# Optimization experiments

Hardware: AMD Instinct MI355X
Metric: run time of the kernel (lower is better)

The kernel has to match this reference:

```python
import jax, jax.numpy as jnp
import numpy as np

B, S, H, DH = 1, 4096, 8, 40  # hardcoded in the original forward
D = H * DH  # 320

def setup_inputs() -> dict:
    key = jax.random.key(0)
    ks = jax.random.split(key, 6)
    s = 1.0 / np.sqrt(D)
    return {
        "x": jax.random.normal(ks[0], (B, S, D), dtype=jnp.float32),
        "Wq": jax.random.normal(ks[1], (D, D), dtype=jnp.float32) * s,
        "Wk": jax.random.normal(ks[2], (D, D), dtype=jnp.float32) * s,
        "Wv": jax.random.normal(ks[3], (D, D), dtype=jnp.float32) * s,
        "Wo": jax.random.normal(ks[4], (D, D), dtype=jnp.float32) * s,
        "bo": jnp.zeros((D,), dtype=jnp.float32),
    }

def reference(x, Wq, Wk, Wv, Wo, bo):
    scale = DH ** (-0.5)
    # nn.Linear(bias=False): y = x @ W^T. context = x (self-attention).
    q = x @ Wq.T
    k = x @ Wk.T
    v = x @ Wv.T
    # split heads: [B,S,D] -> [B*H, S, DH]
    def split_heads(t):
        return t.reshape(B, S, H, DH).transpose(0, 2, 1, 3).reshape(B * H, S, DH)
    q, k, v = split_heads(q), split_heads(k), split_heads(v)
    # fp32 QK^T (original forces float), softmax, AV
    sim = jnp.einsum('bid,bjd->bij', q.astype(jnp.float32), k.astype(jnp.float32)) * scale
    attn = jax.nn.softmax(sim, axis=-1)
    out = jnp.einsum('bij,bjd->bid', attn, v)
    # merge heads: [B*H, S, DH] -> [B, S, D]
    out = out.reshape(B, H, S, DH).transpose(0, 2, 1, 3).reshape(B, S, D)
    return out @ Wo.T + bo
```

## Files before the change

kernel.cpp:

```cpp
#include <hip/hip_runtime.h>
#include <math.h>


#define NS 4096
#define ND 320
#define SCALE2 0.2281101152f
#define HS48 196608
#define VTH 163840
#define XN 1310720

#define KSTR 56
#define VSTR 72
#define VB   3584
#define BUF  7040

typedef __attribute__((ext_vector_type(8))) short bf16x8;
typedef __attribute__((ext_vector_type(16))) float f32x16;

static __device__ __forceinline__ unsigned short f2bru(float f) {
  return (unsigned short)((__builtin_bit_cast(unsigned int, f) + 0x8000u) >> 16);
}
static __device__ __forceinline__ unsigned int pk2ru(float a, float b) {
  unsigned int ua = __builtin_bit_cast(unsigned int, a) + 0x8000u;
  unsigned int ub = __builtin_bit_cast(unsigned int, b) + 0x8000u;
  return __builtin_amdgcn_perm(ub, ua, 0x07060302u);
}
static __device__ __forceinline__ unsigned int pk2t(float a, float b) {
  return __builtin_amdgcn_perm(__builtin_bit_cast(unsigned int, b),
                               __builtin_bit_cast(unsigned int, a), 0x07060302u);
}
static __device__ __forceinline__ float fexp2(float x) {
  return __builtin_amdgcn_exp2f(x);
}
static __device__ __forceinline__ bf16x8 ld8a(const unsigned short* p) {
  return __builtin_bit_cast(bf16x8, *(const uint4*)p);
}
static __device__ __forceinline__ void st16a(unsigned short* p, uint4 v) {
  *(uint4*)p = v;
}
static __device__ __forceinline__ uint4 ld16u(const unsigned short* p) {
  uint2 a = *(const uint2*)p, b = *(const uint2*)(p + 4);
  return make_uint4(a.x, a.y, b.x, b.y);
}
static __device__ __forceinline__ void st16(unsigned short* p, uint4 v) {
  *(uint2*)p = make_uint2(v.x, v.y);
  *(uint2*)(p + 4) = make_uint2(v.z, v.w);
}
static __device__ __forceinline__ int sig32(int q) {
  int s = q >> 4, h2 = (q >> 3) & 1, j = q & 7;
  return (s << 4) | ((j >> 2) << 3) | (h2 << 2) | (j & 3);
}

__global__ __launch_bounds__(256) void proj_qkv_kernel(
    const float* __restrict__ x, const float* __restrict__ Wq,
    const float* __restrict__ Wk, const float* __restrict__ Wv,
    unsigned short* __restrict__ Qp, unsigned short* __restrict__ Kp,
    unsigned short* __restrict__ Vt) {
  const int zi = blockIdx.y;
  const int z = zi / 5;
  const int bnn = (zi - z * 5) * 64;
  const float* W = (z == 0) ? Wq : (z == 1) ? Wk : Wv;
  __shared__ __align__(16) unsigned short As[64 * 88];
  __shared__ __align__(16) unsigned short Bs[64 * 88];
  const int t = threadIdx.x;
  const int w = t >> 6, l = t & 63, l31 = l & 31, hi = l >> 5;
  const int bm = blockIdx.x * 64;
  const int m0 = (w >> 1) * 32, n0 = (w & 1) * 32;
  f32x16 acc = {0,0,0,0,0,0,0,0,0,0,0,0,0,0,0,0};
  const unsigned short* af = As + (m0 + l31) * 88 + hi * 8;
  const unsigned short* bf = Bs + (n0 + l31) * 88 + hi * 8;
  for (int k0 = 0; k0 < ND; k0 += 64) {
    __syncthreads();
#pragma unroll
    for (int i = 0; i < 2; i++) {
      int c = t + i * 256;
      int row = c >> 3, kc = (c & 7) << 3;
      const float* g = x + (bm + row) * ND + k0 + kc;
      float4 v0 = *(const float4*)g, v1 = *(const float4*)(g + 4);
      st16a(As + row * 88 + kc,
            make_uint4(pk2ru(v0.x, v0.y), pk2ru(v0.z, v0.w),
                       pk2ru(v1.x, v1.y), pk2ru(v1.z, v1.w)));
    }
#pragma unroll
    for (int i = 0; i < 2; i++) {
      int c = t + i * 256;
      int row = c >> 3, kc = (c & 7) << 3;
      const float* g = W + (bnn + row) * ND + k0 + kc;
      float4 v0 = *(const float4*)g, v1 = *(const float4*)(g + 4);
      st16a(Bs + row * 88 + kc,
            make_uint4(pk2ru(v0.x, v0.y), pk2ru(v0.z, v0.w),
                       pk2ru(v1.x, v1.y), pk2ru(v1.z, v1.w)));
    }
    __syncthreads();
#pragma unroll
    for (int ks = 0; ks < 4; ks++) {
      acc = __builtin_amdgcn_mfma_f32_32x32x16_bf16(
          ld8a(af + ks * 16), ld8a(bf + ks * 16), acc, 0, 0, 0);
    }
  }
  __syncthreads();
  if (z < 2) {
    unsigned short* Tile = As;
    unsigned short* Y = (z == 0) ? Qp : Kp;
    const float sc = (z == 0) ? SCALE2 : 1.0f;
    const unsigned int padw = (z == 0) ? 0xC200u : 0x3F80u;
#pragma unroll
    for (int r2 = 0; r2 < 16; r2++) {
      int lr = m0 + (r2 & 3) + 8 * (r2 >> 2) + 4 * hi;
      Tile[lr * 68 + n0 + l31] = f2bru(acc[r2] * sc);
    }
    __syncthreads();
#pragma unroll
    for (int i = 0; i < 2; i++) {
      int c = t + i * 256;
      int row = c >> 3, ch = c & 7;
      int j = bnn + ch * 8;
      int h = j / 40, dh = j - h * 40;
      uint4 v = ld16u(Tile + row * 68 + ch * 8);
      st16(Y + h * HS48 + (bm + row) * 48 + dh, v);
      if (dh == 0)
        st16(Y + h * HS48 + (bm + row) * 48 + 40, make_uint4(padw, 0u, 0u, 0u));
    }
  } else {
    unsigned short* Tile = As;
#pragma unroll
    for (int r2 = 0; r2 < 16; r2++) {
      int lr = m0 + (r2 & 3) + 8 * (r2 >> 2) + 4 * hi;
      Tile[(n0 + l31) * 68 + lr] = f2bru(acc[r2]);
    }
    __syncthreads();
#pragma unroll
    for (int i = 0; i < 2; i++) {
      int c = t + i * 256;
      int row = c >> 3, ch = c & 7;
      int j = bnn + row;
      int h = j / 40, dd = j - h * 40;
      uint4 v = ld16u(Tile + row * 68 + ch * 8);
      st16(Vt + h * VTH + dd * NS + bm + ch * 8, v);
    }
  }
}

__global__ __launch_bounds__(256, 4) void attn_kernel(
    const unsigned short* __restrict__ Qp, const unsigned short* __restrict__ Kp,
    const unsigned short* __restrict__ Vt, unsigned short* __restrict__ Op,
    float* __restrict__ Lp) {
  const int b = blockIdx.x;
  const int h = b & 7, ks = (b >> 3) & 3, qt = b >> 5;
  const int t = threadIdx.x;
  const int w = t >> 6, l = t & 63, l31 = l & 31, hi = l >> 5;
  __shared__ __align__(16) unsigned short Lds[2 * BUF];
  for (int i = t; i < 576; i += 256) {
    int bsel = (i >= 288) ? 1 : 0;
    int ui = i - bsel * 288;
    int rr = ui / 36, cc = ui - rr * 36;
    ((unsigned int*)Lds)[bsel * (BUF / 2) + (VB / 2) + (40 + rr) * 36 + cc] =
        (rr == 0 && cc < 32) ? 0x3F803F80u : 0u;
  }

  const int kbase = ks * 1024;
  const int qbase = qt * 128 + w * 32;
  const unsigned short* qp = Qp + h * HS48 + (qbase + l31) * 48 + hi * 8;
  bf16x8 qf0 = *(const bf16x8*)qp;
  bf16x8 qf1 = *(const bf16x8*)(qp + 16);
  bf16x8 qf2 = *(const bf16x8*)(qp + 32);

  const f32x16 Z = {0,0,0,0,0,0,0,0,0,0,0,0,0,0,0,0};
  f32x16 oa0 = Z, oa1 = Z;

  const int id1 = t + 256;
  const bool has2 = (t < 192);
  const int kr0 = t / 6, kc0 = t - kr0 * 6;
  const unsigned short* g0 = Kp + h * HS48 + (kbase + kr0) * 48 + kc0 * 8;
  const int w0 = ((kr0 & 32) | sig32(kr0 & 31)) * KSTR + kc0 * 8;
  const unsigned short* g1;
  int w1, inc1;
  if (id1 < 384) {
    int kr = id1 / 6, kc = id1 - kr * 6;
    g1 = Kp + h * HS48 + (kbase + kr) * 48 + kc * 8;
    w1 = ((kr & 32) | sig32(kr & 31)) * KSTR + kc * 8;
    inc1 = 64 * 48;
  } else {
    int vid = id1 - 384, vr = vid >> 3, vc = vid & 7;
    g1 = Vt + h * VTH + vr * NS + kbase + vc * 8;
    w1 = VB + vr * VSTR + vc * 8;
    inc1 = 64;
  }
  const int vid2 = t + 128;
  const int vr2 = vid2 >> 3, vc2 = vid2 & 7;
  const unsigned short* g2 = Vt + h * VTH + vr2 * NS + kbase + vc2 * 8;
  const int w2 = VB + vr2 * VSTR + vc2 * 8;

  const int rk  = l31 * KSTR + hi * 8;
  const int rv0 = VB + l31 * VSTR + hi * 8;
  const int rv1 = VB + (32 + (l31 & 15)) * VSTR + hi * 8;

  uint4 r0 = *(const uint4*)g0; g0 += 3072;
  uint4 r1 = *(const uint4*)g1; g1 += inc1;
  uint4 r2{};
  if (has2) { r2 = *(const uint4*)g2; g2 += 64; }
  st16a(Lds + w0, r0);
  st16a(Lds + w1, r1);
  if (has2) st16a(Lds + w2, r2);
  r0 = *(const uint4*)g0; g0 += 3072;
  r1 = *(const uint4*)g1; g1 += inc1;
  if (has2) { r2 = *(const uint4*)g2; g2 += 64; }
  __syncthreads();

  for (int it = 0; it < 16; ++it) {
    const int bo = (it & 1) ? BUF : 0;
    const int bn = BUF - bo;
    st16a(Lds + bn + w0, r0);
    st16a(Lds + bn + w1, r1);
    if (has2) st16a(Lds + bn + w2, r2);
    r0 = *(const uint4*)g0; g0 += 3072;
    r1 = *(const uint4*)g1; g1 += inc1;
    if (has2) { r2 = *(const uint4*)g2; g2 += 64; }

    const unsigned short* kf0 = Lds + bo + rk;
    const unsigned short* kf1 = kf0 + 32 * KSTR;
    const unsigned short* vf0 = Lds + bo + rv0;
    const unsigned short* vf1 = Lds + bo + rv1;

    __builtin_amdgcn_s_setprio(1);
    {
      f32x16 s0 = __builtin_amdgcn_mfma_f32_32x32x16_bf16(ld8a(kf0), qf0, Z, 0, 0, 0);
      s0 = __builtin_amdgcn_mfma_f32_32x32x16_bf16(ld8a(kf0 + 16), qf1, s0, 0, 0, 0);
      s0 = __builtin_amdgcn_mfma_f32_32x32x16_bf16(ld8a(kf0 + 32), qf2, s0, 0, 0, 0);
      unsigned int pw[8];
#pragma unroll
      for (int i = 0; i < 8; i++)
        pw[i] = pk2t(fexp2(s0[2 * i]), fexp2(s0[2 * i + 1]));
      bf16x8 pf0 = __builtin_bit_cast(bf16x8, make_uint4(pw[0], pw[1], pw[2], pw[3]));
      bf16x8 pf1 = __builtin_bit_cast(bf16x8, make_uint4(pw[4], pw[5], pw[6], pw[7]));
      oa0 = __builtin_amdgcn_mfma_f32_32x32x16_bf16(pf0, ld8a(vf0), oa0, 0, 0, 0);
      oa1 = __builtin_amdgcn_mfma_f32_32x32x16_bf16(pf0, ld8a(vf1), oa1, 0, 0, 0);
      oa0 = __builtin_amdgcn_mfma_f32_32x32x16_bf16(pf1, ld8a(vf0 + 16), oa0, 0, 0, 0);
      oa1 = __builtin_amdgcn_mfma_f32_32x32x16_bf16(pf1, ld8a(vf1 + 16), oa1, 0, 0, 0);
    }
    {
      f32x16 s1 = __builtin_amdgcn_mfma_f32_32x32x16_bf16(ld8a(kf1), qf0, Z, 0, 0, 0);
      s1 = __builtin_amdgcn_mfma_f32_32x32x16_bf16(ld8a(kf1 + 16), qf1, s1, 0, 0, 0);
      s1 = __builtin_amdgcn_mfma_f32_32x32x16_bf16(ld8a(kf1 + 32), qf2, s1, 0, 0, 0);
      unsigned int pw[8];
#pragma unroll
      for (int i = 0; i < 8; i++)
        pw[i] = pk2t(fexp2(s1[2 * i]), fexp2(s1[2 * i + 1]));
      bf16x8 pf2 = __builtin_bit_cast(bf16x8, make_uint4(pw[0], pw[1], pw[2], pw[3]));
      bf16x8 pf3 = __builtin_bit_cast(bf16x8, make_uint4(pw[4], pw[5], pw[6], pw[7]));
      oa0 = __builtin_amdgcn_mfma_f32_32x32x16_bf16(pf2, ld8a(vf0 + 32), oa0, 0, 0, 0);
      oa1 = __builtin_amdgcn_mfma_f32_32x32x16_bf16(pf2, ld8a(vf1 + 32), oa1, 0, 0, 0);
      oa0 = __builtin_amdgcn_mfma_f32_32x32x16_bf16(pf3, ld8a(vf0 + 48), oa0, 0, 0, 0);
      oa1 = __builtin_amdgcn_mfma_f32_32x32x16_bf16(pf3, ld8a(vf1 + 48), oa1, 0, 0, 0);
    }
    __builtin_amdgcn_s_setprio(0);
    __syncthreads();
  }

  unsigned short* opb = Op + ks * XN + h * 163840;
  float* lpb = Lp + ks * 32768 + h * NS;
#pragma unroll
  for (int r2i = 0; r2i < 16; r2i++) {
    int qr = qbase + (r2i & 3) + 8 * (r2i >> 2) + 4 * hi;
    opb[qr * 40 + l31] = f2bru(oa0[r2i]);
    if (l31 < 8) opb[qr * 40 + 32 + l31] = f2bru(oa1[r2i]);
    if (l31 == 8) lpb[qr] = oa1[r2i];
  }
}

__global__ __launch_bounds__(256) void combine_kernel(
    const unsigned short* __restrict__ Op, const float* __restrict__ Lp,
    unsigned short* __restrict__ Xo) {
  int e = (blockIdx.x * 256 + threadIdx.x) * 2;
  int h = e / 163840;
  int r = e - h * 163840;
  int s = r / 40;
  int dh = r - s * 40;
  float a0 = 0.f, a1 = 0.f, lsum = 0.f;
#pragma unroll
  for (int k = 0; k < 4; k++) {
    unsigned int u = *(const unsigned int*)(Op + k * XN + e);
    a0 += __builtin_bit_cast(float, u << 16);
    a1 += __builtin_bit_cast(float, u & 0xFFFF0000u);
    lsum += Lp[k * 32768 + h * NS + s];
  }
  float inv = 1.0f / lsum;
  *(unsigned int*)(Xo + s * ND + h * 40 + dh) = pk2ru(a0 * inv, a1 * inv);
}

__global__ __launch_bounds__(256) void proj_out_kernel(
    const unsigned short* __restrict__ Xo, const float* __restrict__ Wo,
    const float* __restrict__ bo, float* __restrict__ out) {
  __shared__ __align__(16) unsigned short As[64 * 88];
  __shared__ __align__(16) unsigned short Bs[64 * 88];
  const int t = threadIdx.x;
  const int w = t >> 6, l = t & 63, l31 = l & 31, hi = l >> 5;
  const int bm = blockIdx.x * 64;
  const int bnn = blockIdx.y * 64;
  const int m0 = (w >> 1) * 32, n0 = (w & 1) * 32;
  f32x16 acc = {0,0,0,0,0,0,0,0,0,0,0,0,0,0,0,0};
  const unsigned short* af = As + (m0 + l31) * 88 + hi * 8;
  const unsigned short* bf = Bs + (n0 + l31) * 88 + hi * 8;
  for (int k0 = 0; k0 < ND; k0 += 64) {
    __syncthreads();
#pragma unroll
    for (int i = 0; i < 2; i++) {
      int c = t + i * 256;
      int row = c >> 3, kc = (c & 7) << 3;
      uint4 v = *(const uint4*)(Xo + (bm + row) * ND + k0 + kc);
      st16a(As + row * 88 + kc, v);
    }
#pragma unroll
    for (int i = 0; i < 2; i++) {
      int c = t + i * 256;
      int row = c >> 3, kc = (c & 7) << 3;
      const float* g = Wo + (bnn + row) * ND + k0 + kc;
      float4 v0 = *(const float4*)g, v1 = *(const float4*)(g + 4);
      st16a(Bs + row * 88 + kc,
            make_uint4(pk2ru(v0.x, v0.y), pk2ru(v0.z, v0.w),
                       pk2ru(v1.x, v1.y), pk2ru(v1.z, v1.w)));
    }
    __syncthreads();
#pragma unroll
    for (int ks = 0; ks < 4; ks++) {
      acc = __builtin_amdgcn_mfma_f32_32x32x16_bf16(
          ld8a(af + ks * 16), ld8a(bf + ks * 16), acc, 0, 0, 0);
    }
  }
  const int j = bnn + n0 + l31;
  const float bj = bo[j];
#pragma unroll
  for (int r2 = 0; r2 < 16; r2++) {
    int row = bm + m0 + (r2 & 3) + 8 * (r2 >> 2) + 4 * hi;
    out[row * ND + j] = acc[r2] + bj;
  }
}

extern "C" void kernel_launch(void* const* d_in, const int* in_sizes, int n_in,
                              void* d_out, int out_size, void* d_ws, size_t ws_size,
                              hipStream_t stream) {
  (void)in_sizes; (void)n_in; (void)out_size; (void)ws_size;
  const float* x  = (const float*)d_in[0];
  const float* Wq = (const float*)d_in[1];
  const float* Wk = (const float*)d_in[2];
  const float* Wv = (const float*)d_in[3];
  const float* Wo = (const float*)d_in[4];
  const float* bo = (const float*)d_in[5];
  float* out = (float*)d_out;

  unsigned short* Qp = (unsigned short*)d_ws;
  unsigned short* Kp = Qp + 8 * HS48;
  unsigned short* Vt = Kp + 8 * HS48;
  unsigned short* Xo = Vt + 8 * VTH;
  unsigned short* Op = Xo + XN;
  float* Lp = (float*)(Op + 4 * XN);

  proj_qkv_kernel<<<dim3(64, 15), 256, 0, stream>>>(x, Wq, Wk, Wv, Qp, Kp, Vt);
  attn_kernel<<<dim3(1024), 256, 0, stream>>>(Qp, Kp, Vt, Op, Lp);
  combine_kernel<<<dim3(2560), 256, 0, stream>>>(Op, Lp, Xo);
  proj_out_kernel<<<dim3(64, 5), 256, 0, stream>>>(Xo, Wo, bo, out);
}
```

Before: 123.0 us.

## Process two query tiles per warp to reuse K/V LDS loads in attention

Each attention block now covers 256 query rows instead of 128. Every warp holds two sets of Q fragments and two sets of output accumulators, so each K and V fragment read from LDS feeds both query tiles. The grid is halved to 512 blocks, which halves the total K/V global-to-LDS traffic. In exchange, register pressure roughly doubles, so launch bounds drop from 4 to 2 waves per SIMD, and fewer blocks mean less parallelism for hiding latency.

After: 121.7 us. No clear change (-1.0%).

```diff
diff --git a/kernel.cpp b/kernel.cpp
--- a/kernel.cpp
+++ b/kernel.cpp
@@ -141,7 +141,7 @@
   }
 }
 
-__global__ __launch_bounds__(256, 4) void attn_kernel(
+__global__ __launch_bounds__(256, 2) void attn_kernel(
     const unsigned short* __restrict__ Qp, const unsigned short* __restrict__ Kp,
     const unsigned short* __restrict__ Vt, unsigned short* __restrict__ Op,
     float* __restrict__ Lp) {
@@ -159,14 +159,18 @@
   }
 
   const int kbase = ks * 1024;
-  const int qbase = qt * 128 + w * 32;
+  const int qbase = qt * 256 + w * 32;
   const unsigned short* qp = Qp + h * HS48 + (qbase + l31) * 48 + hi * 8;
-  bf16x8 qf0 = *(const bf16x8*)qp;
-  bf16x8 qf1 = *(const bf16x8*)(qp + 16);
-  bf16x8 qf2 = *(const bf16x8*)(qp + 32);
+  bf16x8 qf0a = *(const bf16x8*)qp;
+  bf16x8 qf1a = *(const bf16x8*)(qp + 16);
+  bf16x8 qf2a = *(const bf16x8*)(qp + 32);
+  const unsigned short* qpb = qp + 128 * 48;
+  bf16x8 qf0b = *(const bf16x8*)qpb;
+  bf16x8 qf1b = *(const bf16x8*)(qpb + 16);
+  bf16x8 qf2b = *(const bf16x8*)(qpb + 32);
 
   const f32x16 Z = {0,0,0,0,0,0,0,0,0,0,0,0,0,0,0,0};
-  f32x16 oa0 = Z, oa1 = Z;
+  f32x16 oa0a = Z, oa1a = Z, oa0b = Z, oa1b = Z;
 
   const int id1 = t + 256;
   const bool has2 = (t < 192);
@@ -218,40 +222,45 @@
     if (has2) { r2 = *(const uint4*)g2; g2 += 64; }
 
     const unsigned short* kf0 = Lds + bo + rk;
-    const unsigned short* kf1 = kf0 + 32 * KSTR;
     const unsigned short* vf0 = Lds + bo + rv0;
     const unsigned short* vf1 = Lds + bo + rv1;
 
     __builtin_amdgcn_s_setprio(1);
-    {
-      f32x16 s0 = __builtin_amdgcn_mfma_f32_32x32x16_bf16(ld8a(kf0), qf0, Z, 0, 0, 0);
-      s0 = __builtin_amdgcn_mfma_f32_32x32x16_bf16(ld8a(kf0 + 16), qf1, s0, 0, 0, 0);
-      s0 = __builtin_amdgcn_mfma_f32_32x32x16_bf16(ld8a(kf0 + 32), qf2, s0, 0, 0, 0);
-      unsigned int pw[8];
+#pragma unroll
+    for (int mt = 0; mt < 2; mt++) {
+      const unsigned short* kf = kf0 + mt * (32 * KSTR);
+      bf16x8 kA = ld8a(kf);
+      bf16x8 kB = ld8a(kf + 16);
+      bf16x8 kC = ld8a(kf + 32);
+      f32x16 sa = __builtin_amdgcn_mfma_f32_32x32x16_bf16(kA, qf0a, Z, 0, 0, 0);
+      sa = __builtin_amdgcn_mfma_f32_32x32x16_bf16(kB, qf1a, sa, 0, 0, 0);
+      sa = __builtin_amdgcn_mfma_f32_32x32x16_bf16(kC, qf2a, sa, 0, 0, 0);
+      f32x16 sb = __builtin_amdgcn_mfma_f32_32x32x16_bf16(kA, qf0b, Z, 0, 0, 0);
+      sb = __builtin_amdgcn_mfma_f32_32x32x16_bf16(kB, qf1b, sb, 0, 0, 0);
+      sb = __builtin_amdgcn_mfma_f32_32x32x16_bf16(kC, qf2b, sb, 0, 0, 0);
+      unsigned int pwa[8], pwb[8];
 #pragma unroll
       for (int i = 0; i < 8; i++)
-        pw[i] = pk2t(fexp2(s0[2 * i]), fexp2(s0[2 * i + 1]));
-      bf16x8 pf0 = __builtin_bit_cast(bf16x8, make_uint4(pw[0], pw[1], pw[2], pw[3]));
-      bf16x8 pf1 = __builtin_bit_cast(bf16x8, make_uint4(pw[4], pw[5], pw[6], pw[7]));
-      oa0 = __builtin_amdgcn_mfma_f32_32x32x16_bf16(pf0, ld8a(vf0), oa0, 0, 0, 0);
-      oa1 = __builtin_amdgcn_mfma_f32_32x32x16_bf16(pf0, ld8a(vf1), oa1, 0, 0, 0);
-      oa0 = __builtin_amdgcn_mfma_f32_32x32x16_bf16(pf1, ld8a(vf0 + 16), oa0, 0, 0, 0);
-      oa1 = __builtin_amdgcn_mfma_f32_32x32x16_bf16(pf1, ld8a(vf1 + 16), oa1, 0, 0, 0);
-    }
-    {
-      f32x16 s1 = __builtin_amdgcn_mfma_f32_32x32x16_bf16(ld8a(kf1), qf0, Z, 0, 0, 0);
-      s1 = __builtin_amdgcn_mfma_f32_32x32x16_bf16(ld8a(kf1 + 16), qf1, s1, 0, 0, 0);
-      s1 = __builtin_amdgcn_mfma_f32_32x32x16_bf16(ld8a(kf1 + 32), qf2, s1, 0, 0, 0);
-      unsigned int pw[8];
+        pwa[i] = pk2t(fexp2(sa[2 * i]), fexp2(sa[2 * i + 1]));
 #pragma unroll
       for (int i = 0; i < 8; i++)
-        pw[i] = pk2t(fexp2(s1[2 * i]), fexp2(s1[2 * i + 1]));
-      bf16x8 pf2 = __builtin_bit_cast(bf16x8, make_uint4(pw[0], pw[1], pw[2], pw[3]));
-      bf16x8 pf3 = __builtin_bit_cast(bf16x8, make_uint4(pw[4], pw[5], pw[6], pw[7]));
-      oa0 = __builtin_amdgcn_mfma_f32_32x32x16_bf16(pf2, ld8a(vf0 + 32), oa0, 0, 0, 0);
-      oa1 = __builtin_amdgcn_mfma_f32_32x32x16_bf16(pf2, ld8a(vf1 + 32), oa1, 0, 0, 0);
-      oa0 = __builtin_amdgcn_mfma_f32_32x32x16_bf16(pf3, ld8a(vf0 + 48), oa0, 0, 0, 0);
-      oa1 = __builtin_amdgcn_mfma_f32_32x32x16_bf16(pf3, ld8a(vf1 + 48), oa1, 0, 0, 0);
+        pwb[i] = pk2t(fexp2(sb[2 * i]), fexp2(sb[2 * i + 1]));
+      bf16x8 pf0a = __builtin_bit_cast(bf16x8, make_uint4(pwa[0], pwa[1], pwa[2], pwa[3]));
+      bf16x8 pf1a = __builtin_bit_cast(bf16x8, make_uint4(pwa[4], pwa[5], pwa[6], pwa[7]));
+      bf16x8 pf0b = __builtin_bit_cast(bf16x8, make_uint4(pwb[0], pwb[1], pwb[2], pwb[3]));
+      bf16x8 pf1b = __builtin_bit_cast(bf16x8, make_uint4(pwb[4], pwb[5], pwb[6], pwb[7]));
+      bf16x8 v0 = ld8a(vf0 + mt * 32);
+      bf16x8 v1 = ld8a(vf1 + mt * 32);
+      bf16x8 v2 = ld8a(vf0 + mt * 32 + 16);
+      bf16x8 v3 = ld8a(vf1 + mt * 32 + 16);
+      oa0a = __builtin_amdgcn_mfma_f32_32x32x16_bf16(pf0a, v0, oa0a, 0, 0, 0);
+      oa1a = __builtin_amdgcn_mfma_f32_32x32x16_bf16(pf0a, v1, oa1a, 0, 0, 0);
+      oa0a = __builtin_amdgcn_mfma_f32_32x32x16_bf16(pf1a, v2, oa0a, 0, 0, 0);
+      oa1a = __builtin_amdgcn_mfma_f32_32x32x16_bf16(pf1a, v3, oa1a, 0, 0, 0);
+      oa0b = __builtin_amdgcn_mfma_f32_32x32x16_bf16(pf0b, v0, oa0b, 0, 0, 0);
+      oa1b = __builtin_amdgcn_mfma_f32_32x32x16_bf16(pf0b, v1, oa1b, 0, 0, 0);
+      oa0b = __builtin_amdgcn_mfma_f32_32x32x16_bf16(pf1b, v2, oa0b, 0, 0, 0);
+      oa1b = __builtin_amdgcn_mfma_f32_32x32x16_bf16(pf1b, v3, oa1b, 0, 0, 0);
     }
     __builtin_amdgcn_s_setprio(0);
     __syncthreads();
@@ -262,9 +271,13 @@
 #pragma unroll
   for (int r2i = 0; r2i < 16; r2i++) {
     int qr = qbase + (r2i & 3) + 8 * (r2i >> 2) + 4 * hi;
-    opb[qr * 40 + l31] = f2bru(oa0[r2i]);
-    if (l31 < 8) opb[qr * 40 + 32 + l31] = f2bru(oa1[r2i]);
-    if (l31 == 8) lpb[qr] = oa1[r2i];
+    opb[qr * 40 + l31] = f2bru(oa0a[r2i]);
+    if (l31 < 8) opb[qr * 40 + 32 + l31] = f2bru(oa1a[r2i]);
+    if (l31 == 8) lpb[qr] = oa1a[r2i];
+    int qr2 = qr + 128;
+    opb[qr2 * 40 + l31] = f2bru(oa0b[r2i]);
+    if (l31 < 8) opb[qr2 * 40 + 32 + l31] = f2bru(oa1b[r2i]);
+    if (l31 == 8) lpb[qr2] = oa1b[r2i];
   }
 }
 
@@ -356,7 +369,7 @@
   float* Lp = (float*)(Op + 4 * XN);
 
   proj_qkv_kernel<<<dim3(64, 15), 256, 0, stream>>>(x, Wq, Wk, Wv, Qp, Kp, Vt);
-  attn_kernel<<<dim3(1024), 256, 0, stream>>>(Qp, Kp, Vt, Op, Lp);
+  attn_kernel<<<dim3(512), 256, 0, stream>>>(Qp, Kp, Vt, Op, Lp);
   combine_kernel<<<dim3(2560), 256, 0, stream>>>(Op, Lp, Xo);
   proj_out_kernel<<<dim3(64, 5), 256, 0, stream>>>(Xo, Wo, bo, out);
 }
```

## Halve attention KV split, double-buffer QKV projection, vectorize combine

Applied to the files above, without the earlier changes.

The attention kernel now splits keys into 2 chunks of 2048 instead of 4 of 1024. This halves the grid to 512 blocks and the partial outputs the combine step must read. The combine kernel processes 8 elements per thread with 16-byte loads. The QKV projection GEMM gains double-buffered LDS with register prefetch of the next k-tile, removing one barrier per iteration. The trade-off is fewer attention blocks on a large GPU, so occupancy may drop, and twice the LDS in the projection kernel.

Result: faster. 119.3 us (-3.0%).

```diff
diff --git a/kernel.cpp b/kernel.cpp
--- a/kernel.cpp
+++ b/kernel.cpp
@@ -60,47 +60,67 @@
   const int z = zi / 5;
   const int bnn = (zi - z * 5) * 64;
   const float* W = (z == 0) ? Wq : (z == 1) ? Wk : Wv;
-  __shared__ __align__(16) unsigned short As[64 * 88];
-  __shared__ __align__(16) unsigned short Bs[64 * 88];
+  __shared__ __align__(16) unsigned short As[2][64 * 88];
+  __shared__ __align__(16) unsigned short Bs[2][64 * 88];
   const int t = threadIdx.x;
   const int w = t >> 6, l = t & 63, l31 = l & 31, hi = l >> 5;
   const int bm = blockIdx.x * 64;
   const int m0 = (w >> 1) * 32, n0 = (w & 1) * 32;
   f32x16 acc = {0,0,0,0,0,0,0,0,0,0,0,0,0,0,0,0};
-  const unsigned short* af = As + (m0 + l31) * 88 + hi * 8;
-  const unsigned short* bf = Bs + (n0 + l31) * 88 + hi * 8;
-  for (int k0 = 0; k0 < ND; k0 += 64) {
-    __syncthreads();
-#pragma unroll
-    for (int i = 0; i < 2; i++) {
-      int c = t + i * 256;
-      int row = c >> 3, kc = (c & 7) << 3;
-      const float* g = x + (bm + row) * ND + k0 + kc;
-      float4 v0 = *(const float4*)g, v1 = *(const float4*)(g + 4);
-      st16a(As + row * 88 + kc,
-            make_uint4(pk2ru(v0.x, v0.y), pk2ru(v0.z, v0.w),
-                       pk2ru(v1.x, v1.y), pk2ru(v1.z, v1.w)));
-    }
-#pragma unroll
-    for (int i = 0; i < 2; i++) {
-      int c = t + i * 256;
-      int row = c >> 3, kc = (c & 7) << 3;
-      const float* g = W + (bnn + row) * ND + k0 + kc;
-      float4 v0 = *(const float4*)g, v1 = *(const float4*)(g + 4);
-      st16a(Bs + row * 88 + kc,
-            make_uint4(pk2ru(v0.x, v0.y), pk2ru(v0.z, v0.w),
-                       pk2ru(v1.x, v1.y), pk2ru(v1.z, v1.w)));
-    }
-    __syncthreads();
-#pragma unroll
-    for (int ks = 0; ks < 4; ks++) {
+  const int afo = (m0 + l31) * 88 + hi * 8;
+  const int bfo = (n0 + l31) * 88 + hi * 8;
+  const int row0 = t >> 3, row1 = row0 + 32, kc = (t & 7) << 3;
+  const float* xb = x + (bm + row0) * ND + kc;
+  const float* xb1 = x + (bm + row1) * ND + kc;
+  const float* Wb = W + (bnn + row0) * ND + kc;
+  const float* Wb1 = W + (bnn + row1) * ND + kc;
+  const int so0 = row0 * 88 + kc, so1 = row1 * 88 + kc;
+
+  float4 a00, a01, a10, a11, b00, b01, b10, b11;
+#define PQ_LOAD(K)                                                   \
+  do {                                                               \
+    a00 = *(const float4*)(xb + (K));  a01 = *(const float4*)(xb + (K) + 4);  \
+    a10 = *(const float4*)(xb1 + (K)); a11 = *(const float4*)(xb1 + (K) + 4); \
+    b00 = *(const float4*)(Wb + (K));  b01 = *(const float4*)(Wb + (K) + 4);  \
+    b10 = *(const float4*)(Wb1 + (K)); b11 = *(const float4*)(Wb1 + (K) + 4); \
+  } while (0)
+#define PQ_STORE(BUFI)                                               \
+  do {                                                               \
+    st16a(&As[BUFI][so0], make_uint4(pk2ru(a00.x, a00.y), pk2ru(a00.z, a00.w), \
+                                     pk2ru(a01.x, a01.y), pk2ru(a01.z, a01.w))); \
+    st16a(&As[BUFI][so1], make_uint4(pk2ru(a10.x, a10.y), pk2ru(a10.z, a10.w), \
+                                     pk2ru(a11.x, a11.y), pk2ru(a11.z, a11.w))); \
+    st16a(&Bs[BUFI][so0], make_uint4(pk2ru(b00.x, b00.y), pk2ru(b00.z, b00.w), \
+                                     pk2ru(b01.x, b01.y), pk2ru(b01.z, b01.w))); \
+    st16a(&Bs[BUFI][so1], make_uint4(pk2ru(b10.x, b10.y), pk2ru(b10.z, b10.w), \
+                                     pk2ru(b11.x, b11.y), pk2ru(b11.z, b11.w))); \
+  } while (0)
+
+  PQ_LOAD(0);
+  PQ_STORE(0);
+  PQ_LOAD(64);
+  __syncthreads();
+#pragma unroll
+  for (int it = 0; it < 5; ++it) {
+    const int cur = it & 1, nxt = cur ^ 1;
+    if (it < 4) PQ_STORE(nxt);
+    {
+      int kp = (it + 2) * 64;
+      if (kp >= ND) kp = 0;
+      PQ_LOAD(kp);
+    }
+#pragma unroll
+    for (int kk = 0; kk < 4; kk++) {
       acc = __builtin_amdgcn_mfma_f32_32x32x16_bf16(
-          ld8a(af + ks * 16), ld8a(bf + ks * 16), acc, 0, 0, 0);
-    }
-  }
-  __syncthreads();
+          ld8a(&As[cur][afo + kk * 16]), ld8a(&Bs[cur][bfo + kk * 16]), acc, 0, 0, 0);
+    }
+    __syncthreads();
+  }
+#undef PQ_LOAD
+#undef PQ_STORE
+
+  unsigned short* Tile = &As[0][0];
   if (z < 2) {
-    unsigned short* Tile = As;
     unsigned short* Y = (z == 0) ? Qp : Kp;
     const float sc = (z == 0) ? SCALE2 : 1.0f;
     const unsigned int padw = (z == 0) ? 0xC200u : 0x3F80u;
@@ -122,7 +142,6 @@
         st16(Y + h * HS48 + (bm + row) * 48 + 40, make_uint4(padw, 0u, 0u, 0u));
     }
   } else {
-    unsigned short* Tile = As;
 #pragma unroll
     for (int r2 = 0; r2 < 16; r2++) {
       int lr = m0 + (r2 & 3) + 8 * (r2 >> 2) + 4 * hi;
@@ -146,7 +165,7 @@
     const unsigned short* __restrict__ Vt, unsigned short* __restrict__ Op,
     float* __restrict__ Lp) {
   const int b = blockIdx.x;
-  const int h = b & 7, ks = (b >> 3) & 3, qt = b >> 5;
+  const int h = b & 7, ks = (b >> 3) & 1, qt = b >> 4;
   const int t = threadIdx.x;
   const int w = t >> 6, l = t & 63, l31 = l & 31, hi = l >> 5;
   __shared__ __align__(16) unsigned short Lds[2 * BUF];
@@ -158,7 +177,7 @@
         (rr == 0 && cc < 32) ? 0x3F803F80u : 0u;
   }
 
-  const int kbase = ks * 1024;
+  const int kbase = ks * 2048;
   const int qbase = qt * 128 + w * 32;
   const unsigned short* qp = Qp + h * HS48 + (qbase + l31) * 48 + hi * 8;
   bf16x8 qf0 = *(const bf16x8*)qp;
@@ -207,7 +226,7 @@
   if (has2) { r2 = *(const uint4*)g2; g2 += 64; }
   __syncthreads();
 
-  for (int it = 0; it < 16; ++it) {
+  for (int it = 0; it < 32; ++it) {
     const int bo = (it & 1) ? BUF : 0;
     const int bn = BUF - bo;
     st16a(Lds + bn + w0, r0);
@@ -271,21 +290,30 @@
 __global__ __launch_bounds__(256) void combine_kernel(
     const unsigned short* __restrict__ Op, const float* __restrict__ Lp,
     unsigned short* __restrict__ Xo) {
-  int e = (blockIdx.x * 256 + threadIdx.x) * 2;
+  int e = (blockIdx.x * 256 + threadIdx.x) * 8;
   int h = e / 163840;
   int r = e - h * 163840;
   int s = r / 40;
   int dh = r - s * 40;
-  float a0 = 0.f, a1 = 0.f, lsum = 0.f;
-#pragma unroll
-  for (int k = 0; k < 4; k++) {
-    unsigned int u = *(const unsigned int*)(Op + k * XN + e);
-    a0 += __builtin_bit_cast(float, u << 16);
-    a1 += __builtin_bit_cast(float, u & 0xFFFF0000u);
+  float a[8] = {0, 0, 0, 0, 0, 0, 0, 0};
+  float lsum = 0.f;
+#pragma unroll
+  for (int k = 0; k < 2; k++) {
+    uint4 u = *(const uint4*)(Op + k * XN + e);
+    a[0] += __builtin_bit_cast(float, u.x << 16);
+    a[1] += __builtin_bit_cast(float, u.x & 0xFFFF0000u);
+    a[2] += __builtin_bit_cast(float, u.y << 16);
+    a[3] += __builtin_bit_cast(float, u.y & 0xFFFF0000u);
+    a[4] += __builtin_bit_cast(float, u.z << 16);
+    a[5] += __builtin_bit_cast(float, u.z & 0xFFFF0000u);
+    a[6] += __builtin_bit_cast(float, u.w << 16);
+    a[7] += __builtin_bit_cast(float, u.w & 0xFFFF0000u);
     lsum += Lp[k * 32768 + h * NS + s];
   }
   float inv = 1.0f / lsum;
-  *(unsigned int*)(Xo + s * ND + h * 40 + dh) = pk2ru(a0 * inv, a1 * inv);
+  *(uint4*)(Xo + s * ND + h * 40 + dh) =
+      make_uint4(pk2ru(a[0] * inv, a[1] * inv), pk2ru(a[2] * inv, a[3] * inv),
+                 pk2ru(a[4] * inv, a[5] * inv), pk2ru(a[6] * inv, a[7] * inv));
 }
 
 __global__ __launch_bounds__(256) void proj_out_kernel(
@@ -353,10 +381,10 @@
   unsigned short* Vt = Kp + 8 * HS48;
   unsigned short* Xo = Vt + 8 * VTH;
   unsigned short* Op = Xo + XN;
-  float* Lp = (float*)(Op + 4 * XN);
+  float* Lp = (float*)(Op + 2 * XN);
 
   proj_qkv_kernel<<<dim3(64, 15), 256, 0, stream>>>(x, Wq, Wk, Wv, Qp, Kp, Vt);
-  attn_kernel<<<dim3(1024), 256, 0, stream>>>(Qp, Kp, Vt, Op, Lp);
-  combine_kernel<<<dim3(2560), 256, 0, stream>>>(Op, Lp, Xo);
+  attn_kernel<<<dim3(512), 256, 0, stream>>>(Qp, Kp, Vt, Op, Lp);
+  combine_kernel<<<dim3(640), 256, 0, stream>>>(Op, Lp, Xo);
   proj_out_kernel<<<dim3(64, 5), 256, 0, stream>>>(Xo, Wo, bo, out);
 }
```
